# Kernel tuning notes

Hardware: AMD Instinct MI355X
Metric: run time of the kernel (lower is better)

Reference implementation:

```python
import jax, jax.numpy as jnp
import numpy as np

N = 150000      # nodes per branch
E = 2400000     # edges per branch (avg degree 16)
G = 128         # graphs in batch
F_IN, H, EMB = 3, 128, 512
BN_EPS = 1e-5


def setup_inputs() -> dict:
    key = jax.random.key(0)
    ks = jax.random.split(key, 24)
    inp = {
        "x1": jax.random.normal(ks[0], (N, F_IN), jnp.float32),
        "edge_index1": jax.random.randint(ks[1], (2, E), 0, N, jnp.int32),
        "batch1": jnp.sort(jax.random.randint(ks[2], (N,), 0, G, jnp.int32)),
        "x2": jax.random.normal(ks[3], (N, F_IN), jnp.float32),
        "edge_index2": jax.random.randint(ks[4], (2, E), 0, N, jnp.int32),
        "batch2": jnp.sort(jax.random.randint(ks[5], (N,), 0, G, jnp.int32)),
        # GCNConv weights (PyG: out = norm-agg(x @ W) + b), shared (siamese)
        "W1": jax.random.normal(ks[6], (F_IN, H), jnp.float32) / np.sqrt(F_IN),
        "b1": jnp.zeros((H,), jnp.float32),
        "W2": jax.random.normal(ks[7], (H, H), jnp.float32) / np.sqrt(H),
        "b2": jnp.zeros((H,), jnp.float32),
        "W3": jax.random.normal(ks[8], (H, H), jnp.float32) / np.sqrt(H),
        "b3": jnp.zeros((H,), jnp.float32),
        # BatchNorm affine params
        "g1": jnp.ones((H,), jnp.float32), "be1": jnp.zeros((H,), jnp.float32),
        "g2": jnp.ones((H,), jnp.float32), "be2": jnp.zeros((H,), jnp.float32),
        # projection MLP
        "Wp1": jax.random.normal(ks[9], (H, H), jnp.float32) / np.sqrt(H),
        "bp1": jnp.zeros((H,), jnp.float32),
        "Wp2": jax.random.normal(ks[10], (H, EMB), jnp.float32) / np.sqrt(H),
        "bp2": jnp.zeros((EMB,), jnp.float32),
    }
    return inp


def gcn_conv(x, edge_index, W, b):
    """PyG GCNConv: add self-loops, symmetric D^-1/2 (A+I) D^-1/2 normalization."""
    n = x.shape[0]
    loop = jnp.arange(n, dtype=edge_index.dtype)
    src = jnp.concatenate([edge_index[0], loop])
    dst = jnp.concatenate([edge_index[1], loop])
    deg = jax.ops.segment_sum(jnp.ones_like(dst, jnp.float32), dst, num_segments=n)
    dinv = jnp.where(deg > 0, jax.lax.rsqrt(deg), 0.0)
    norm = dinv[src] * dinv[dst]                      # [E+N]
    h = x @ W                                         # [N,H] dense transform first
    msg = h[src] * norm[:, None]                      # gather + scale
    out = jax.ops.segment_sum(msg, dst, num_segments=n)  # scatter-add
    return out + b


def batch_norm(x, gamma, beta):
    mu = jnp.mean(x, axis=0)
    var = jnp.mean(jnp.square(x - mu), axis=0)  # biased, training-mode stats
    return (x - mu) * jax.lax.rsqrt(var + BN_EPS) * gamma + beta


def global_mean_pool(x, batch, num_graphs):
    sums = jax.ops.segment_sum(x, batch, num_segments=num_graphs)
    cnt = jax.ops.segment_sum(jnp.ones((x.shape[0],), x.dtype), batch, num_segments=num_graphs)
    return sums / jnp.maximum(cnt, 1.0)[:, None]


def forward_once(x, edge_index, batch, W1, b1, W2, b2, W3, b3, g1, be1, g2, be2, Wp1, bp1, Wp2, bp2):
    x = jax.nn.relu(batch_norm(gcn_conv(x, edge_index, W1, b1), g1, be1))
    x = jax.nn.relu(batch_norm(gcn_conv(x, edge_index, W2, b2), g2, be2))
    x = gcn_conv(x, edge_index, W3, b3)
    x = global_mean_pool(x, batch, G)                 # [G,H]
    x = jax.nn.relu(x @ Wp1 + bp1) @ Wp2 + bp2        # [G,EMB]
    nrm = jnp.linalg.norm(x, axis=1, keepdims=True)
    return x / jnp.maximum(nrm, 1e-12)                # F.normalize(p=2, dim=1)


def reference(x1, edge_index1, batch1, x2, edge_index2, batch2,
              W1, b1, W2, b2, W3, b3, g1, be1, g2, be2, Wp1, bp1, Wp2, bp2):
    params = (W1, b1, W2, b2, W3, b3, g1, be1, g2, be2, Wp1, bp1, Wp2, bp2)
    out1 = forward_once(x1, edge_index1, batch1, *params)
    out2 = forward_once(x2, edge_index2, batch2, *params)
    return (out1, out2)
```

## Files before the change

### kernel.cpp

```cpp
#include <hip/hip_runtime.h>
#include <math.h>

#define BUCKET_SHIFT 8
#define BUCKET_MASK 255
#define MAXBUCK 640
#define TILE 8192

typedef __attribute__((ext_vector_type(8))) short bf16x8;
typedef __attribute__((ext_vector_type(4))) float f32x4;

__device__ inline float bf_lo(unsigned u) { return __uint_as_float(u << 16); }
__device__ inline float bf_hi(unsigned u) { return __uint_as_float(u & 0xffff0000u); }
__device__ inline float bf2f(unsigned short s) { return __uint_as_float((unsigned)s << 16); }
__device__ inline unsigned short f2bf(float f) {
  unsigned u = __float_as_uint(f);
  return (unsigned short)((u + 0x7fffu + ((u >> 16) & 1u)) >> 16);
}
__device__ inline void acc8(float* a, uint4 v) {
  a[0] += bf_lo(v.x); a[1] += bf_hi(v.x);
  a[2] += bf_lo(v.y); a[3] += bf_hi(v.y);
  a[4] += bf_lo(v.z); a[5] += bf_hi(v.z);
  a[6] += bf_lo(v.w); a[7] += bf_hi(v.w);
}
__device__ inline unsigned pack2(float a, float b) {
  return (unsigned)f2bf(a) | ((unsigned)f2bf(b) << 16);
}

__global__ void zero_u32(unsigned int* __restrict__ p, int n) {
  int i = blockIdx.x * blockDim.x + threadIdx.x;
  if (i < n) p[i] = 0u;
}

__global__ __launch_bounds__(256) void bucket_count(const int* __restrict__ dst0,
                                                    const int* __restrict__ dst1,
                                                    int* __restrict__ bcnt, int e, int nbuck) {
  int br = blockIdx.y;
  const int* dst = br ? dst1 : dst0;
  bcnt += (size_t)br * nbuck;
  __shared__ int lc[MAXBUCK];
  for (int i = threadIdx.x; i < nbuck; i += 256) lc[i] = 0;
  __syncthreads();
  for (int i = blockIdx.x * blockDim.x + threadIdx.x; i < e; i += gridDim.x * blockDim.x)
    atomicAdd(&lc[dst[i] >> BUCKET_SHIFT], 1);
  __syncthreads();
  for (int i = threadIdx.x; i < nbuck; i += 256)
    if (lc[i]) atomicAdd(&bcnt[i], lc[i]);
}

__global__ __launch_bounds__(1024) void bucket_scan(const int* __restrict__ bcnt,
                                                    int* __restrict__ bbase,
                                                    int* __restrict__ bcur, int nbuck) {
  int br = blockIdx.y;
  bcnt += (size_t)br * nbuck;
  bbase += (size_t)br * (nbuck + 1);
  bcur += (size_t)br * nbuck;
  __shared__ int s[1024];
  int t = threadIdx.x;
  int v = (t < nbuck) ? bcnt[t] : 0;
  s[t] = v;
  __syncthreads();
  for (int off = 1; off < 1024; off <<= 1) {
    int u = (t >= off) ? s[t - off] : 0;
    __syncthreads();
    s[t] += u;
    __syncthreads();
  }
  int excl = s[t] - v;
  if (t < nbuck) {
    bbase[t] = excl;
    bcur[t] = excl;
  } else if (t == nbuck) {
    bbase[t] = excl;
  }
}

__global__ __launch_bounds__(256) void bucket_scatter(const int* __restrict__ src0,
                                                      const int* __restrict__ dst0,
                                                      const int* __restrict__ src1,
                                                      const int* __restrict__ dst1,
                                                      int* __restrict__ bcur,
                                                      int* __restrict__ bucketed,
                                                      int e, int nbuck) {
  int br = blockIdx.y;
  const int* src = br ? src1 : src0;
  const int* dst = br ? dst1 : dst0;
  bcur += (size_t)br * nbuck;
  bucketed += (size_t)br * e;
  __shared__ int lcnt[MAXBUCK], gb[MAXBUCK];
  int t = threadIdx.x;
  int tile0 = blockIdx.x * TILE;
  int tn = min(TILE, e - tile0);
  for (int i = t; i < nbuck; i += 256) lcnt[i] = 0;
  __syncthreads();
  for (int i = t; i < tn; i += 256)
    atomicAdd(&lcnt[dst[tile0 + i] >> BUCKET_SHIFT], 1);
  __syncthreads();
  for (int i = t; i < nbuck; i += 256) {
    int c = lcnt[i];
    gb[i] = c ? atomicAdd(&bcur[i], c) : 0;
  }
  __syncthreads();
  for (int i = t; i < nbuck; i += 256) lcnt[i] = 0;
  __syncthreads();
  for (int i = t; i < tn; i += 256) {
    int d = dst[tile0 + i];
    int s = src[tile0 + i];
    int b = d >> BUCKET_SHIFT;
    int r = atomicAdd(&lcnt[b], 1);
    bucketed[gb[b] + r] = (s << 8) | (d & BUCKET_MASK);
  }
}

__global__ __launch_bounds__(256) void bucket_to_csr(const int* __restrict__ bucketed,
                                                     const int* __restrict__ bbase,
                                                     int* __restrict__ rp,
                                                     float* __restrict__ dinv,
                                                     int* __restrict__ csr,
                                                     int n, int e, int nbuck) {
  int br = blockIdx.y;
  bucketed += (size_t)br * e;
  bbase += (size_t)br * (nbuck + 1);
  rp += (size_t)br * (n + 1);
  dinv += (size_t)br * n;
  csr += (size_t)br * e;
  __shared__ int lcnt[256], lrp[256];
  int b = blockIdx.x, t = threadIdx.x;
  int n0 = b << BUCKET_SHIFT;
  int base = bbase[b];
  int cnt_e = bbase[b + 1] - base;
  lcnt[t] = 0;
  __syncthreads();
  for (int i = t; i < cnt_e; i += 256)
    atomicAdd(&lcnt[bucketed[base + i] & BUCKET_MASK], 1);
  __syncthreads();
  int v = lcnt[t];
  lrp[t] = v;
  __syncthreads();
  for (int off = 1; off < 256; off <<= 1) {
    int u = (t >= off) ? lrp[t - off] : 0;
    __syncthreads();
    lrp[t] += u;
    __syncthreads();
  }
  int excl = lrp[t] - v;
  int node = n0 + t;
  if (node < n) {
    rp[node] = base + excl;
    dinv[node] = rsqrtf((float)v + 1.0f);
  }
  if (b == nbuck - 1 && t == 0) rp[n] = e;
  lrp[t] = excl;
  lcnt[t] = 0;
  __syncthreads();
  for (int i = t; i < cnt_e; i += 256) {
    int ed = bucketed[base + i];
    int li = ed & BUCKET_MASK;
    int pos = atomicAdd(&lcnt[li], 1);
    csr[base + lrp[li] + pos] = (int)(((unsigned)ed) >> 8);
  }
}

__global__ void graph_bounds(const int* __restrict__ batch0, const int* __restrict__ batch1,
                             int* __restrict__ gstart, int n, int g) {
  int br = blockIdx.y;
  const int* batch = br ? batch1 : batch0;
  gstart += (size_t)br * (g + 1);
  int i = blockIdx.x * blockDim.x + threadIdx.x;
  if (i >= n) return;
  int b = batch[i];
  int bp = (i == 0) ? -1 : batch[i - 1];
  for (int k = bp + 1; k <= b; ++k) gstart[k] = i;
  if (i == n - 1)
    for (int k = b + 1; k <= g; ++k) gstart[k] = n;
}

__global__ void xs_scale(const float* __restrict__ x0, const float* __restrict__ x1,
                         const float* __restrict__ dinv, float4* __restrict__ xs, int n) {
  int br = blockIdx.y;
  const float* x = br ? x1 : x0;
  dinv += (size_t)br * n;
  xs += (size_t)br * n;
  int i = blockIdx.x * blockDim.x + threadIdx.x;
  if (i >= n) return;
  float d = dinv[i];
  xs[i] = make_float4(x[3 * (size_t)i] * d, x[3 * (size_t)i + 1] * d,
                      x[3 * (size_t)i + 2] * d, d);
}

__global__ __launch_bounds__(256) void agg_f3(const float4* __restrict__ xs,
                                              const int* __restrict__ rp,
                                              const int* __restrict__ csr,
                                              const float* __restrict__ dinv,
                                              float4* __restrict__ out,
                                              float* __restrict__ mpart, int n, int e, int nb3) {
  int br = blockIdx.y;
  xs += (size_t)br * n;
  rp += (size_t)br * (n + 1);
  csr += (size_t)br * e;
  dinv += (size_t)br * n;
  out += (size_t)br * n;
  mpart += (size_t)br * nb3 * 9;
  int i = blockIdx.x * blockDim.x + threadIdx.x;
  int t = threadIdx.x;
  float a0 = 0.f, a1 = 0.f, a2 = 0.f;
  if (i < n) {
    float4 self = xs[i];
    a0 = self.x; a1 = self.y; a2 = self.z;
    int e0 = rp[i], e1 = rp[i + 1];
    int ee = e0;
    for (; ee + 4 <= e1; ee += 4) {
      int s0 = csr[ee], s1 = csr[ee + 1], s2 = csr[ee + 2], s3 = csr[ee + 3];
      float4 v0 = xs[s0], v1 = xs[s1], v2 = xs[s2], v3 = xs[s3];
      a0 += (v0.x + v1.x) + (v2.x + v3.x);
      a1 += (v0.y + v1.y) + (v2.y + v3.y);
      a2 += (v0.z + v1.z) + (v2.z + v3.z);
    }
    for (; ee < e1; ++ee) {
      float4 v = xs[csr[ee]];
      a0 += v.x; a1 += v.y; a2 += v.z;
    }
    float d = dinv[i];
    a0 *= d; a1 *= d; a2 *= d;
    out[i] = make_float4(a0, a1, a2, 0.f);
  }
  float loc[9] = {a0, a1, a2, a0 * a0, a0 * a1, a0 * a2, a1 * a1, a1 * a2, a2 * a2};
  __shared__ float red[256];
  for (int q = 0; q < 9; ++q) {
    red[t] = loc[q];
    __syncthreads();
    for (int s = 128; s > 0; s >>= 1) {
      if (t < s) red[t] += red[t + s];
      __syncthreads();
    }
    if (t == 0) mpart[blockIdx.x * 9 + q] = red[0];
    __syncthreads();
  }
}

__global__ void bnprep1(const float* __restrict__ mpart, int nblk,
                        const float* __restrict__ W1, const float* __restrict__ b1,
                        const float* __restrict__ g1, const float* __restrict__ be1,
                        float invn, float4* __restrict__ W1r, float2* __restrict__ prm) {
  int br = blockIdx.y;
  mpart += (size_t)br * nblk * 9;
  W1r += (size_t)br * 128;
  prm += (size_t)br * 128;
  __shared__ float red[256];
  __shared__ float sm[9];
  int t = threadIdx.x;
  float loc[9] = {0.f, 0.f, 0.f, 0.f, 0.f, 0.f, 0.f, 0.f, 0.f};
  for (int i = t; i < nblk; i += 256)
#pragma unroll
    for (int q = 0; q < 9; ++q) loc[q] += mpart[i * 9 + q];
  for (int q = 0; q < 9; ++q) {
    red[t] = loc[q];
    __syncthreads();
    for (int s = 128; s > 0; s >>= 1) {
      if (t < s) red[t] += red[t + s];
      __syncthreads();
    }
    if (t == 0) sm[q] = red[0] * invn;
    __syncthreads();
  }
  if (t < 128) {
    float w0 = W1[t], w1 = W1[128 + t], w2 = W1[256 + t], b = b1[t];
    float mu0 = sm[0] * w0 + sm[1] * w1 + sm[2] * w2;
    float q2 = w0 * w0 * sm[3] + w1 * w1 * sm[6] + w2 * w2 * sm[8]
             + 2.f * (w0 * w1 * sm[4] + w0 * w2 * sm[5] + w1 * w2 * sm[7]);
    float var = q2 - mu0 * mu0;
    float sc = rsqrtf(fmaxf(var, 0.f) + 1e-5f) * g1[t];
    float mu = mu0 + b;
    W1r[t] = make_float4(w0, w1, w2, b);
    prm[t] = make_float2(sc, be1[t] - mu * sc);
  }
}

__global__ void lin1_fused(const float4* __restrict__ ag, const float4* __restrict__ W1r,
                           const float2* __restrict__ prm, unsigned short* __restrict__ out,
                           int n) {
  int br = blockIdx.y;
  ag += (size_t)br * n;
  W1r += (size_t)br * 128;
  prm += (size_t)br * 128;
  out += (size_t)br * n * 128;
  int idx = blockIdx.x * blockDim.x + threadIdx.x;
  if (idx >= n * 128) return;
  int node = idx >> 7, f = idx & 127;
  float4 a = ag[node];
  float4 w = W1r[f];
  float2 p = prm[f];
  float v = a.x * w.x + a.y * w.y + a.z * w.z + w.w;
  v = v * p.x + p.y;
  out[idx] = f2bf(fmaxf(v, 0.f));
}

__global__ void wsplit2(const float* __restrict__ W2, const float* __restrict__ W3,
                        unsigned short* __restrict__ Wf2, unsigned short* __restrict__ Wf3) {
  const float* W = blockIdx.y ? W3 : W2;
  unsigned short* Wf = blockIdx.y ? Wf3 : Wf2;
  int i = blockIdx.x * 256 + threadIdx.x;
  if (i >= 128 * 128) return;
  int k = i >> 7, f = i & 127;
  float w = W[i];
  unsigned short hi = f2bf(w);
  float hif = __uint_as_float((unsigned)hi << 16);
  unsigned short lo = f2bf(w - hif);
  int NT = f >> 4, l15 = f & 15, ks = k >> 5, lg = (k >> 3) & 3, j = k & 7;
  int lane = lg * 16 + l15;
  size_t base = ((size_t)(NT * 4 + ks) * 64 + lane) * 8 + j;
  Wf[base] = hi;
  Wf[16384 + base] = lo;
}

template <int BN>
__global__ __launch_bounds__(256) void gemm_mfma_t(const unsigned short* __restrict__ Abf,
                                                   const unsigned short* __restrict__ Wf,
                                                   const float* __restrict__ dinv,
                                                   const float2* __restrict__ prm,
                                                   unsigned short* __restrict__ C, int n) {
  int br = blockIdx.y;
  Abf += (size_t)br * n * 128;
  dinv += (size_t)br * n;
  C += (size_t)br * n * 128;
  if (BN) prm += (size_t)br * 128;
  const int t = threadIdx.x;
  const int wave = t >> 6, lane = t & 63;
  const int l15 = lane & 15, lg = lane >> 4;
  const int row0 = blockIdx.x * 128 + wave * 32;
  const int n0 = row0 + l15, n1 = row0 + 16 + l15;
  const bf16x8* wfr = (const bf16x8*)Wf;
  f32x4 acc[8][2] = {};
#pragma unroll
  for (int ks = 0; ks < 4; ++ks) {
    int k0 = ks * 32 + lg * 8;
    bf16x8 nf0 = {}, nf1 = {};
    if (n0 < n) nf0 = *(const bf16x8*)&Abf[(size_t)n0 * 128 + k0];
    if (n1 < n) nf1 = *(const bf16x8*)&Abf[(size_t)n1 * 128 + k0];
    if (BN) {
      float4 pa = *(const float4*)&prm[k0];
      float4 pb = *(const float4*)&prm[k0 + 2];
      float4 pc = *(const float4*)&prm[k0 + 4];
      float4 pd = *(const float4*)&prm[k0 + 6];
      float scv[8] = {pa.x, pa.z, pb.x, pb.z, pc.x, pc.z, pd.x, pd.z};
      float ofv[8] = {pa.y, pa.w, pb.y, pb.w, pc.y, pc.w, pd.y, pd.w};
#pragma unroll
      for (int j = 0; j < 8; ++j) {
        float x0 = fmaxf(bf2f((unsigned short)nf0[j]) * scv[j] + ofv[j], 0.f);
        float x1 = fmaxf(bf2f((unsigned short)nf1[j]) * scv[j] + ofv[j], 0.f);
        nf0[j] = (short)f2bf(x0);
        nf1[j] = (short)f2bf(x1);
      }
    }
#pragma unroll
    for (int NT = 0; NT < 8; ++NT) {
      bf16x8 wh = wfr[(NT * 4 + ks) * 64 + lane];
      bf16x8 wl = wfr[2048 + (NT * 4 + ks) * 64 + lane];
      acc[NT][0] = __builtin_amdgcn_mfma_f32_16x16x32_bf16(wh, nf0, acc[NT][0], 0, 0, 0);
      acc[NT][0] = __builtin_amdgcn_mfma_f32_16x16x32_bf16(wl, nf0, acc[NT][0], 0, 0, 0);
      acc[NT][1] = __builtin_amdgcn_mfma_f32_16x16x32_bf16(wh, nf1, acc[NT][1], 0, 0, 0);
      acc[NT][1] = __builtin_amdgcn_mfma_f32_16x16x32_bf16(wl, nf1, acc[NT][1], 0, 0, 0);
    }
  }
  float sc0 = (n0 < n) ? dinv[n0] : 0.f;
  float sc1 = (n1 < n) ? dinv[n1] : 0.f;
#pragma unroll
  for (int ng = 0; ng < 2; ++ng) {
    int node = (ng == 0) ? n0 : n1;
    float sc = (ng == 0) ? sc0 : sc1;
    if (node < n) {
#pragma unroll
      for (int NT = 0; NT < 8; ++NT) {
        ushort4 o;
        o.x = f2bf(acc[NT][ng][0] * sc);
        o.y = f2bf(acc[NT][ng][1] * sc);
        o.z = f2bf(acc[NT][ng][2] * sc);
        o.w = f2bf(acc[NT][ng][3] * sc);
        *(ushort4*)&C[(size_t)node * 128 + NT * 16 + lg * 4] = o;
      }
    }
  }
}

__global__ __launch_bounds__(256) void agg128_l2(const unsigned short* __restrict__ h,
                                                 const int* __restrict__ rp,
                                                 const int* __restrict__ csr,
                                                 const float* __restrict__ dinv,
                                                 const float* __restrict__ bias,
                                                 unsigned short* __restrict__ outb,
                                                 float* __restrict__ mpart, int n, int e,
                                                 int nagg) {
  int br = blockIdx.y;
  h += (size_t)br * n * 128;
  rp += (size_t)br * (n + 1);
  csr += (size_t)br * e;
  dinv += (size_t)br * n;
  outb += (size_t)br * n * 128;
  mpart += (size_t)br * nagg * 256;
  int t = threadIdx.x;
  int node = blockIdx.x * 16 + (t >> 4);
  int lane = t & 15;
  bool valid = node < n;
  const uint4* hp = (const uint4*)h;
  float acc[8] = {0.f};
  if (valid) {
    acc8(acc, hp[(size_t)node * 16 + lane]);
    int e0 = rp[node], e1 = rp[node + 1];
    int ee = e0;
    for (; ee + 8 <= e1; ee += 8) {
      int s0 = csr[ee],     s1 = csr[ee + 1], s2 = csr[ee + 2], s3 = csr[ee + 3];
      int s4 = csr[ee + 4], s5 = csr[ee + 5], s6 = csr[ee + 6], s7 = csr[ee + 7];
      uint4 v0 = hp[(size_t)s0 * 16 + lane];
      uint4 v1 = hp[(size_t)s1 * 16 + lane];
      uint4 v2 = hp[(size_t)s2 * 16 + lane];
      uint4 v3 = hp[(size_t)s3 * 16 + lane];
      uint4 v4 = hp[(size_t)s4 * 16 + lane];
      uint4 v5 = hp[(size_t)s5 * 16 + lane];
      uint4 v6 = hp[(size_t)s6 * 16 + lane];
      uint4 v7 = hp[(size_t)s7 * 16 + lane];
      acc8(acc, v0); acc8(acc, v1); acc8(acc, v2); acc8(acc, v3);
      acc8(acc, v4); acc8(acc, v5); acc8(acc, v6); acc8(acc, v7);
    }
    for (; ee + 4 <= e1; ee += 4) {
      int s0 = csr[ee], s1 = csr[ee + 1], s2 = csr[ee + 2], s3 = csr[ee + 3];
      uint4 v0 = hp[(size_t)s0 * 16 + lane];
      uint4 v1 = hp[(size_t)s1 * 16 + lane];
      uint4 v2 = hp[(size_t)s2 * 16 + lane];
      uint4 v3 = hp[(size_t)s3 * 16 + lane];
      acc8(acc, v0); acc8(acc, v1); acc8(acc, v2); acc8(acc, v3);
    }
    for (; ee < e1; ++ee) acc8(acc, hp[(size_t)csr[ee] * 16 + lane]);
  }
  float v[8], sq[8];
  if (valid) {
    float dd = dinv[node];
    float4 bb0 = *(const float4*)&bias[lane * 8];
    float4 bb1 = *(const float4*)&bias[lane * 8 + 4];
    v[0] = acc[0] * dd + bb0.x; v[1] = acc[1] * dd + bb0.y;
    v[2] = acc[2] * dd + bb0.z; v[3] = acc[3] * dd + bb0.w;
    v[4] = acc[4] * dd + bb1.x; v[5] = acc[5] * dd + bb1.y;
    v[6] = acc[6] * dd + bb1.z; v[7] = acc[7] * dd + bb1.w;
    uint4 o;
    o.x = pack2(v[0], v[1]); o.y = pack2(v[2], v[3]);
    o.z = pack2(v[4], v[5]); o.w = pack2(v[6], v[7]);
    *(uint4*)&outb[(size_t)node * 128 + lane * 8] = o;
  } else {
#pragma unroll
    for (int j = 0; j < 8; ++j) v[j] = 0.f;
  }
#pragma unroll
  for (int j = 0; j < 8; ++j) sq[j] = v[j] * v[j];
#pragma unroll
  for (int j = 0; j < 8; ++j) {
    v[j] += __shfl_xor(v[j], 16);  v[j] += __shfl_xor(v[j], 32);
    sq[j] += __shfl_xor(sq[j], 16); sq[j] += __shfl_xor(sq[j], 32);
  }
  __shared__ float sred[4][16][16];
  int wave = t >> 6, wl = t & 63;
  if (wl < 16) {
#pragma unroll
    for (int j = 0; j < 8; ++j) {
      sred[wave][wl][j] = v[j];
      sred[wave][wl][8 + j] = sq[j];
    }
  }
  __syncthreads();
  {
    int f = t & 127;
    int j = (f & 7) + ((t >> 7) << 3);
    float s = sred[0][f >> 3][j] + sred[1][f >> 3][j]
            + sred[2][f >> 3][j] + sred[3][f >> 3][j];
    mpart[(size_t)blockIdx.x * 256 + t] = s;
  }
}

__global__ __launch_bounds__(256) void bnred1(const float* __restrict__ mpart, int nblk,
                                              float* __restrict__ spart) {
  int br = blockIdx.y;
  mpart += (size_t)br * nblk * 256;
  spart += (size_t)br * 128 * 256;
  int t = threadIdx.x, b = blockIdx.x;
  float loc = 0.f;
  for (int i = b; i < nblk; i += 128) loc += mpart[(size_t)i * 256 + t];
  spart[b * 256 + t] = loc;
}

__global__ void bnprep2(const float* __restrict__ spart,
                        const float* __restrict__ gam, const float* __restrict__ bet,
                        float invn, float2* __restrict__ prm) {
  int br = blockIdx.y;
  spart += (size_t)br * 128 * 256;
  prm += (size_t)br * 128;
  int t = threadIdx.x;
  float loc = 0.f;
  for (int i = 0; i < 128; ++i) loc += spart[i * 256 + t];
  __shared__ float sm[256];
  sm[t] = loc;
  __syncthreads();
  if (t < 128) {
    float mu = sm[t] * invn;
    float var = sm[128 + t] * invn - mu * mu;
    float sc = rsqrtf(fmaxf(var, 0.f) + 1e-5f) * gam[t];
    prm[t] = make_float2(sc, bet[t] - mu * sc);
  }
}

__global__ __launch_bounds__(256) void agg128_l3(const unsigned short* __restrict__ h,
                                                 const int* __restrict__ rp,
                                                 const int* __restrict__ csr,
                                                 const float* __restrict__ dinv,
                                                 const float* __restrict__ bias,
                                                 unsigned short* __restrict__ outb,
                                                 int n, int e) {
  int br = blockIdx.y;
  h += (size_t)br * n * 128;
  rp += (size_t)br * (n + 1);
  csr += (size_t)br * e;
  dinv += (size_t)br * n;
  outb += (size_t)br * n * 128;
  int node = blockIdx.x * 16 + (threadIdx.x >> 4);
  int lane = threadIdx.x & 15;
  if (node >= n) return;
  const uint4* hp = (const uint4*)h;
  float acc[8] = {0.f};
  acc8(acc, hp[(size_t)node * 16 + lane]);
  int e0 = rp[node], e1 = rp[node + 1];
  int ee = e0;
  for (; ee + 8 <= e1; ee += 8) {
    int s0 = csr[ee],     s1 = csr[ee + 1], s2 = csr[ee + 2], s3 = csr[ee + 3];
    int s4 = csr[ee + 4], s5 = csr[ee + 5], s6 = csr[ee + 6], s7 = csr[ee + 7];
    uint4 v0 = hp[(size_t)s0 * 16 + lane];
    uint4 v1 = hp[(size_t)s1 * 16 + lane];
    uint4 v2 = hp[(size_t)s2 * 16 + lane];
    uint4 v3 = hp[(size_t)s3 * 16 + lane];
    uint4 v4 = hp[(size_t)s4 * 16 + lane];
    uint4 v5 = hp[(size_t)s5 * 16 + lane];
    uint4 v6 = hp[(size_t)s6 * 16 + lane];
    uint4 v7 = hp[(size_t)s7 * 16 + lane];
    acc8(acc, v0); acc8(acc, v1); acc8(acc, v2); acc8(acc, v3);
    acc8(acc, v4); acc8(acc, v5); acc8(acc, v6); acc8(acc, v7);
  }
  for (; ee + 4 <= e1; ee += 4) {
    int s0 = csr[ee], s1 = csr[ee + 1], s2 = csr[ee + 2], s3 = csr[ee + 3];
    uint4 v0 = hp[(size_t)s0 * 16 + lane];
    uint4 v1 = hp[(size_t)s1 * 16 + lane];
    uint4 v2 = hp[(size_t)s2 * 16 + lane];
    uint4 v3 = hp[(size_t)s3 * 16 + lane];
    acc8(acc, v0); acc8(acc, v1); acc8(acc, v2); acc8(acc, v3);
  }
  for (; ee < e1; ++ee) acc8(acc, hp[(size_t)csr[ee] * 16 + lane]);
  float dd = dinv[node];
  float4 bb0 = *(const float4*)&bias[lane * 8];
  float4 bb1 = *(const float4*)&bias[lane * 8 + 4];
  uint4 o;
  o.x = pack2(acc[0] * dd + bb0.x, acc[1] * dd + bb0.y);
  o.y = pack2(acc[2] * dd + bb0.z, acc[3] * dd + bb0.w);
  o.z = pack2(acc[4] * dd + bb1.x, acc[5] * dd + bb1.y);
  o.w = pack2(acc[6] * dd + bb1.z, acc[7] * dd + bb1.w);
  *(uint4*)&outb[(size_t)node * 128 + lane * 8] = o;
}

__global__ void pool_partial_bf16(const unsigned short* __restrict__ z,
                                  const int* __restrict__ gstart,
                                  float* __restrict__ pooled, int n, int g) {
  int br = blockIdx.y;
  z += (size_t)br * n * 128;
  gstart += (size_t)br * (g + 1);
  pooled += (size_t)br * g * 128;
  int gg = blockIdx.x >> 3, p = blockIdx.x & 7;
  int t = threadIdx.x;
  int f = t & 127, half = t >> 7;
  int beg = gstart[gg], end = gstart[gg + 1];
  float s = 0.f;
  for (int idx = beg + p * 2 + half; idx < end; idx += 16)
    s += bf2f(z[(size_t)idx * 128 + f]);
  __shared__ float ls[256];
  ls[t] = s;
  __syncthreads();
  if (half == 0) atomicAdd(&pooled[gg * 128 + f], s + ls[t + 128]);
}

__global__ void mlp_kernel(const float* __restrict__ pooled, const int* __restrict__ gstart,
                           const float* __restrict__ Wp1, const float* __restrict__ bp1,
                           const float* __restrict__ Wp2, const float* __restrict__ bp2,
                           float* __restrict__ out, int g) {
  int br = blockIdx.y;
  pooled += (size_t)br * g * 128;
  gstart += (size_t)br * (g + 1);
  out += (size_t)br * g * 512;
  int gg = blockIdx.x, t = threadIdx.x;
  __shared__ float pv[128], hid[128], ov[512], red[256];
  if (t < 128) {
    float cntf = (float)(gstart[gg + 1] - gstart[gg]);
    pv[t] = pooled[gg * 128 + t] / fmaxf(cntf, 1.0f);
  }
  __syncthreads();
  if (t < 128) {
    float a = bp1[t];
    for (int k = 0; k < 128; ++k) a += pv[k] * Wp1[k * 128 + t];
    hid[t] = fmaxf(a, 0.0f);
  }
  __syncthreads();
  for (int o = t; o < 512; o += 256) {
    float a = bp2[o];
    for (int k = 0; k < 128; ++k) a += hid[k] * Wp2[k * 512 + o];
    ov[o] = a;
  }
  __syncthreads();
  red[t] = ov[t] * ov[t] + ov[t + 256] * ov[t + 256];
  __syncthreads();
  for (int sdt = 128; sdt > 0; sdt >>= 1) {
    if (t < sdt) red[t] += red[t + sdt];
    __syncthreads();
  }
  float inv = 1.0f / fmaxf(sqrtf(red[0]), 1e-12f);
  for (int o = t; o < 512; o += 256) out[(size_t)gg * 512 + o] = ov[o] * inv;
}

extern "C" void kernel_launch(void* const* d_in, const int* in_sizes, int n_in,
                              void* d_out, int out_size, void* d_ws, size_t ws_size,
                              hipStream_t stream) {
  const int N = in_sizes[0] / 3;
  const int E = in_sizes[1] / 2;
  const int G = out_size / (2 * 512);
  const int NBUCK = (N + BUCKET_MASK) >> BUCKET_SHIFT;
  const int NB3 = (N + 255) / 256;
  const int NAGG = (N + 15) / 16;

  char* w = (char*)d_ws;
  auto alloc = [&](size_t bytes) -> void* {
    void* p = (void*)w;
    w += (bytes + 255) & ~(size_t)255;
    return p;
  };
  unsigned short* Abf      = (unsigned short*)alloc(2 * (size_t)N * 128 * 2);
  unsigned short* Bh       = (unsigned short*)alloc(2 * (size_t)N * 128 * 2);
  float*          dinv     = (float*)alloc(2 * (size_t)N * 4);
  float4*         xs       = (float4*)alloc(2 * (size_t)N * 16);
  float4*         ag0      = (float4*)alloc(2 * (size_t)N * 16);
  int*            rp       = (int*)alloc(2 * (size_t)(N + 1) * 4);
  int*            csr      = (int*)alloc(2 * (size_t)E * 4);
  int*            bucketed = (int*)alloc(2 * (size_t)E * 4);
  int*            bcnt     = (int*)alloc(2 * (size_t)NBUCK * 4);
  int*            bbase    = (int*)alloc(2 * (size_t)(NBUCK + 1) * 4);
  int*            bcur     = (int*)alloc(2 * (size_t)NBUCK * 4);
  int*            gstart   = (int*)alloc(2 * (size_t)(G + 1) * 4);
  float*          pooled   = (float*)alloc(2 * (size_t)G * 128 * 4);
  unsigned short* Wf2      = (unsigned short*)alloc(2 * 128 * 128 * 2);
  unsigned short* Wf3      = (unsigned short*)alloc(2 * 128 * 128 * 2);
  float*          mpart    = (float*)alloc(2 * (size_t)NB3 * 9 * 4);
  float*          mpart2   = (float*)alloc(2 * (size_t)NAGG * 256 * 4);
  float*          spart    = (float*)alloc(2 * (size_t)128 * 256 * 4);
  float4*         W1r      = (float4*)alloc(2 * 128 * 16);
  float2*         prm1     = (float2*)alloc(2 * 128 * 8);
  float2*         prm2     = (float2*)alloc(2 * 128 * 8);

  const float* x0    = (const float*)d_in[0];
  const int*   ei0   = (const int*)d_in[1];
  const int*   bat0  = (const int*)d_in[2];
  const float* x1    = (const float*)d_in[3];
  const int*   ei1   = (const int*)d_in[4];
  const int*   bat1  = (const int*)d_in[5];
  const float* W1  = (const float*)d_in[6];
  const float* b1  = (const float*)d_in[7];
  const float* W2  = (const float*)d_in[8];
  const float* b2  = (const float*)d_in[9];
  const float* W3  = (const float*)d_in[10];
  const float* b3  = (const float*)d_in[11];
  const float* g1  = (const float*)d_in[12];
  const float* be1 = (const float*)d_in[13];
  const float* g2  = (const float*)d_in[14];
  const float* be2 = (const float*)d_in[15];
  const float* Wp1 = (const float*)d_in[16];
  const float* bp1 = (const float*)d_in[17];
  const float* Wp2 = (const float*)d_in[18];
  const float* bp2 = (const float*)d_in[19];

  const int* src0 = ei0;
  const int* dst0 = ei0 + E;
  const int* src1 = ei1;
  const int* dst1 = ei1 + E;
  float* outp = (float*)d_out;

  const int TB = 256;
  const int NTILE = (E + TILE - 1) / TILE;
  const float invn = 1.0f / (float)N;

  wsplit2<<<dim3(64, 2), TB, 0, stream>>>(W2, W3, Wf2, Wf3);

  zero_u32<<<(2 * NBUCK + TB - 1) / TB, TB, 0, stream>>>((unsigned*)bcnt, 2 * NBUCK);
  bucket_count<<<dim3(256, 2), TB, 0, stream>>>(dst0, dst1, bcnt, E, NBUCK);
  bucket_scan<<<dim3(1, 2), 1024, 0, stream>>>(bcnt, bbase, bcur, NBUCK);
  bucket_scatter<<<dim3(NTILE, 2), TB, 0, stream>>>(src0, dst0, src1, dst1, bcur, bucketed, E, NBUCK);
  bucket_to_csr<<<dim3(NBUCK, 2), TB, 0, stream>>>(bucketed, bbase, rp, dinv, csr, N, E, NBUCK);

  graph_bounds<<<dim3((N + TB - 1) / TB, 2), TB, 0, stream>>>(bat0, bat1, gstart, N, G);

  xs_scale<<<dim3((N + TB - 1) / TB, 2), TB, 0, stream>>>(x0, x1, dinv, xs, N);
  agg_f3<<<dim3(NB3, 2), TB, 0, stream>>>(xs, rp, csr, dinv, ag0, mpart, N, E, NB3);
  bnprep1<<<dim3(1, 2), TB, 0, stream>>>(mpart, NB3, W1, b1, g1, be1, invn, W1r, prm1);
  lin1_fused<<<dim3((N * 128 + TB - 1) / TB, 2), TB, 0, stream>>>(ag0, W1r, prm1, Abf, N);

  gemm_mfma_t<0><<<dim3((N + 127) / 128, 2), TB, 0, stream>>>(Abf, Wf2, dinv, nullptr, Bh, N);
  agg128_l2<<<dim3(NAGG, 2), TB, 0, stream>>>(Bh, rp, csr, dinv, b2, Abf, mpart2, N, E, NAGG);
  bnred1<<<dim3(128, 2), TB, 0, stream>>>(mpart2, NAGG, spart);
  bnprep2<<<dim3(1, 2), TB, 0, stream>>>(spart, g2, be2, invn, prm2);

  gemm_mfma_t<1><<<dim3((N + 127) / 128, 2), TB, 0, stream>>>(Abf, Wf3, dinv, prm2, Bh, N);
  agg128_l3<<<dim3(NAGG, 2), TB, 0, stream>>>(Bh, rp, csr, dinv, b3, Abf, N, E);

  zero_u32<<<(2 * G * 128 + TB - 1) / TB, TB, 0, stream>>>((unsigned*)pooled, 2 * G * 128);
  pool_partial_bf16<<<dim3(G * 8, 2), TB, 0, stream>>>(Abf, gstart, pooled, N, G);
  mlp_kernel<<<dim3(G, 2), TB, 0, stream>>>(pooled, gstart, Wp1, bp1, Wp2, bp2, outp, G);
}
```

Measured before the change: 828.5 us.

## Fuse layer-1 linear+BN into GEMM prologue and pooling into layer-3 aggregation

Drops the standalone lin1_fused kernel. The layer-2 GEMM now rebuilds its bf16 input on the fly from the 3-wide aggregated features, W1 and the BN parameters, so the N×128 bf16 intermediate is never written or read back. The layer-3 aggregation kernel now does the mean-pool sums itself: it reduces node rows per graph in LDS and issues atomicAdds, which removes the write of the final node features and the separate pooling pass. In exchange there are more atomics on the pooled buffer and extra per-element ALU work inside the GEMM prologue.

```diff
diff --git a/kernel.cpp b/kernel.cpp
--- a/kernel.cpp
+++ b/kernel.cpp
@@ -275,25 +275,6 @@
   }
 }
 
-__global__ void lin1_fused(const float4* __restrict__ ag, const float4* __restrict__ W1r,
-                           const float2* __restrict__ prm, unsigned short* __restrict__ out,
-                           int n) {
-  int br = blockIdx.y;
-  ag += (size_t)br * n;
-  W1r += (size_t)br * 128;
-  prm += (size_t)br * 128;
-  out += (size_t)br * n * 128;
-  int idx = blockIdx.x * blockDim.x + threadIdx.x;
-  if (idx >= n * 128) return;
-  int node = idx >> 7, f = idx & 127;
-  float4 a = ag[node];
-  float4 w = W1r[f];
-  float2 p = prm[f];
-  float v = a.x * w.x + a.y * w.y + a.z * w.z + w.w;
-  v = v * p.x + p.y;
-  out[idx] = f2bf(fmaxf(v, 0.f));
-}
-
 __global__ void wsplit2(const float* __restrict__ W2, const float* __restrict__ W3,
                         unsigned short* __restrict__ Wf2, unsigned short* __restrict__ Wf3) {
   const float* W = blockIdx.y ? W3 : W2;
@@ -312,31 +293,39 @@
   Wf[16384 + base] = lo;
 }
 
-template <int BN>
+template <int MODE>
 __global__ __launch_bounds__(256) void gemm_mfma_t(const unsigned short* __restrict__ Abf,
+                                                   const float4* __restrict__ ag0,
+                                                   const float4* __restrict__ W1r,
                                                    const unsigned short* __restrict__ Wf,
                                                    const float* __restrict__ dinv,
                                                    const float2* __restrict__ prm,
                                                    unsigned short* __restrict__ C, int n) {
   int br = blockIdx.y;
-  Abf += (size_t)br * n * 128;
+  if (MODE == 1) Abf += (size_t)br * n * 128;
+  if (MODE == 2) { ag0 += (size_t)br * n; W1r += (size_t)br * 128; }
   dinv += (size_t)br * n;
   C += (size_t)br * n * 128;
-  if (BN) prm += (size_t)br * 128;
+  prm += (size_t)br * 128;
   const int t = threadIdx.x;
   const int wave = t >> 6, lane = t & 63;
   const int l15 = lane & 15, lg = lane >> 4;
   const int row0 = blockIdx.x * 128 + wave * 32;
   const int n0 = row0 + l15, n1 = row0 + 16 + l15;
   const bf16x8* wfr = (const bf16x8*)Wf;
+  float4 a0v = make_float4(0.f, 0.f, 0.f, 0.f), a1v = a0v;
+  if (MODE == 2) {
+    if (n0 < n) a0v = ag0[n0];
+    if (n1 < n) a1v = ag0[n1];
+  }
   f32x4 acc[8][2] = {};
 #pragma unroll
   for (int ks = 0; ks < 4; ++ks) {
     int k0 = ks * 32 + lg * 8;
     bf16x8 nf0 = {}, nf1 = {};
-    if (n0 < n) nf0 = *(const bf16x8*)&Abf[(size_t)n0 * 128 + k0];
-    if (n1 < n) nf1 = *(const bf16x8*)&Abf[(size_t)n1 * 128 + k0];
-    if (BN) {
+    if (MODE == 1) {
+      if (n0 < n) nf0 = *(const bf16x8*)&Abf[(size_t)n0 * 128 + k0];
+      if (n1 < n) nf1 = *(const bf16x8*)&Abf[(size_t)n1 * 128 + k0];
       float4 pa = *(const float4*)&prm[k0];
       float4 pb = *(const float4*)&prm[k0 + 2];
       float4 pc = *(const float4*)&prm[k0 + 4];
@@ -349,6 +338,17 @@
         float x1 = fmaxf(bf2f((unsigned short)nf1[j]) * scv[j] + ofv[j], 0.f);
         nf0[j] = (short)f2bf(x0);
         nf1[j] = (short)f2bf(x1);
+      }
+    } else {
+#pragma unroll
+      for (int j = 0; j < 8; ++j) {
+        int f = k0 + j;
+        float4 wv = W1r[f];
+        float2 p = prm[f];
+        float x0 = (a0v.x * wv.x + a0v.y * wv.y + a0v.z * wv.z + wv.w) * p.x + p.y;
+        float x1 = (a1v.x * wv.x + a1v.y * wv.y + a1v.z * wv.z + wv.w) * p.x + p.y;
+        nf0[j] = (short)f2bf(fmaxf(x0, 0.f));
+        nf1[j] = (short)f2bf(fmaxf(x1, 0.f));
       }
     }
 #pragma unroll
@@ -504,79 +504,98 @@
   }
 }
 
-__global__ __launch_bounds__(256) void agg128_l3(const unsigned short* __restrict__ h,
-                                                 const int* __restrict__ rp,
-                                                 const int* __restrict__ csr,
-                                                 const float* __restrict__ dinv,
-                                                 const float* __restrict__ bias,
-                                                 unsigned short* __restrict__ outb,
-                                                 int n, int e) {
+__global__ __launch_bounds__(256) void agg128_l3_pool(const unsigned short* __restrict__ h,
+                                                      const int* __restrict__ rp,
+                                                      const int* __restrict__ csr,
+                                                      const float* __restrict__ dinv,
+                                                      const float* __restrict__ bias,
+                                                      const int* __restrict__ batch0,
+                                                      const int* __restrict__ batch1,
+                                                      float* __restrict__ pooled,
+                                                      int n, int e, int g) {
   int br = blockIdx.y;
   h += (size_t)br * n * 128;
   rp += (size_t)br * (n + 1);
   csr += (size_t)br * e;
   dinv += (size_t)br * n;
-  outb += (size_t)br * n * 128;
-  int node = blockIdx.x * 16 + (threadIdx.x >> 4);
-  int lane = threadIdx.x & 15;
-  if (node >= n) return;
+  const int* batch = br ? batch1 : batch0;
+  pooled += (size_t)br * g * 128;
+  int t = threadIdx.x;
+  int node = blockIdx.x * 16 + (t >> 4);
+  int lane = t & 15;
+  bool valid = node < n;
   const uint4* hp = (const uint4*)h;
   float acc[8] = {0.f};
-  acc8(acc, hp[(size_t)node * 16 + lane]);
-  int e0 = rp[node], e1 = rp[node + 1];
-  int ee = e0;
-  for (; ee + 8 <= e1; ee += 8) {
-    int s0 = csr[ee],     s1 = csr[ee + 1], s2 = csr[ee + 2], s3 = csr[ee + 3];
-    int s4 = csr[ee + 4], s5 = csr[ee + 5], s6 = csr[ee + 6], s7 = csr[ee + 7];
-    uint4 v0 = hp[(size_t)s0 * 16 + lane];
-    uint4 v1 = hp[(size_t)s1 * 16 + lane];
-    uint4 v2 = hp[(size_t)s2 * 16 + lane];
-    uint4 v3 = hp[(size_t)s3 * 16 + lane];
-    uint4 v4 = hp[(size_t)s4 * 16 + lane];
-    uint4 v5 = hp[(size_t)s5 * 16 + lane];
-    uint4 v6 = hp[(size_t)s6 * 16 + lane];
-    uint4 v7 = hp[(size_t)s7 * 16 + lane];
-    acc8(acc, v0); acc8(acc, v1); acc8(acc, v2); acc8(acc, v3);
-    acc8(acc, v4); acc8(acc, v5); acc8(acc, v6); acc8(acc, v7);
-  }
-  for (; ee + 4 <= e1; ee += 4) {
-    int s0 = csr[ee], s1 = csr[ee + 1], s2 = csr[ee + 2], s3 = csr[ee + 3];
-    uint4 v0 = hp[(size_t)s0 * 16 + lane];
-    uint4 v1 = hp[(size_t)s1 * 16 + lane];
-    uint4 v2 = hp[(size_t)s2 * 16 + lane];
-    uint4 v3 = hp[(size_t)s3 * 16 + lane];
-    acc8(acc, v0); acc8(acc, v1); acc8(acc, v2); acc8(acc, v3);
-  }
-  for (; ee < e1; ++ee) acc8(acc, hp[(size_t)csr[ee] * 16 + lane]);
-  float dd = dinv[node];
-  float4 bb0 = *(const float4*)&bias[lane * 8];
-  float4 bb1 = *(const float4*)&bias[lane * 8 + 4];
-  uint4 o;
-  o.x = pack2(acc[0] * dd + bb0.x, acc[1] * dd + bb0.y);
-  o.y = pack2(acc[2] * dd + bb0.z, acc[3] * dd + bb0.w);
-  o.z = pack2(acc[4] * dd + bb1.x, acc[5] * dd + bb1.y);
-  o.w = pack2(acc[6] * dd + bb1.z, acc[7] * dd + bb1.w);
-  *(uint4*)&outb[(size_t)node * 128 + lane * 8] = o;
-}
-
-__global__ void pool_partial_bf16(const unsigned short* __restrict__ z,
-                                  const int* __restrict__ gstart,
-                                  float* __restrict__ pooled, int n, int g) {
-  int br = blockIdx.y;
-  z += (size_t)br * n * 128;
-  gstart += (size_t)br * (g + 1);
-  pooled += (size_t)br * g * 128;
-  int gg = blockIdx.x >> 3, p = blockIdx.x & 7;
-  int t = threadIdx.x;
-  int f = t & 127, half = t >> 7;
-  int beg = gstart[gg], end = gstart[gg + 1];
-  float s = 0.f;
-  for (int idx = beg + p * 2 + half; idx < end; idx += 16)
-    s += bf2f(z[(size_t)idx * 128 + f]);
-  __shared__ float ls[256];
-  ls[t] = s;
-  __syncthreads();
-  if (half == 0) atomicAdd(&pooled[gg * 128 + f], s + ls[t + 128]);
+  if (valid) {
+    acc8(acc, hp[(size_t)node * 16 + lane]);
+    int e0 = rp[node], e1 = rp[node + 1];
+    int ee = e0;
+    for (; ee + 8 <= e1; ee += 8) {
+      int s0 = csr[ee],     s1 = csr[ee + 1], s2 = csr[ee + 2], s3 = csr[ee + 3];
+      int s4 = csr[ee + 4], s5 = csr[ee + 5], s6 = csr[ee + 6], s7 = csr[ee + 7];
+      uint4 v0 = hp[(size_t)s0 * 16 + lane];
+      uint4 v1 = hp[(size_t)s1 * 16 + lane];
+      uint4 v2 = hp[(size_t)s2 * 16 + lane];
+      uint4 v3 = hp[(size_t)s3 * 16 + lane];
+      uint4 v4 = hp[(size_t)s4 * 16 + lane];
+      uint4 v5 = hp[(size_t)s5 * 16 + lane];
+      uint4 v6 = hp[(size_t)s6 * 16 + lane];
+      uint4 v7 = hp[(size_t)s7 * 16 + lane];
+      acc8(acc, v0); acc8(acc, v1); acc8(acc, v2); acc8(acc, v3);
+      acc8(acc, v4); acc8(acc, v5); acc8(acc, v6); acc8(acc, v7);
+    }
+    for (; ee + 4 <= e1; ee += 4) {
+      int s0 = csr[ee], s1 = csr[ee + 1], s2 = csr[ee + 2], s3 = csr[ee + 3];
+      uint4 v0 = hp[(size_t)s0 * 16 + lane];
+      uint4 v1 = hp[(size_t)s1 * 16 + lane];
+      uint4 v2 = hp[(size_t)s2 * 16 + lane];
+      uint4 v3 = hp[(size_t)s3 * 16 + lane];
+      acc8(acc, v0); acc8(acc, v1); acc8(acc, v2); acc8(acc, v3);
+    }
+    for (; ee < e1; ++ee) acc8(acc, hp[(size_t)csr[ee] * 16 + lane]);
+  }
+  __shared__ float lds[16][128];
+  __shared__ int lgid[16];
+  int ng = t >> 4;
+  if (valid) {
+    float dd = dinv[node];
+    float4 bb0 = *(const float4*)&bias[lane * 8];
+    float4 bb1 = *(const float4*)&bias[lane * 8 + 4];
+    float w0 = bf2f(f2bf(acc[0] * dd + bb0.x));
+    float w1 = bf2f(f2bf(acc[1] * dd + bb0.y));
+    float w2 = bf2f(f2bf(acc[2] * dd + bb0.z));
+    float w3 = bf2f(f2bf(acc[3] * dd + bb0.w));
+    float w4 = bf2f(f2bf(acc[4] * dd + bb1.x));
+    float w5 = bf2f(f2bf(acc[5] * dd + bb1.y));
+    float w6 = bf2f(f2bf(acc[6] * dd + bb1.z));
+    float w7 = bf2f(f2bf(acc[7] * dd + bb1.w));
+    lds[ng][lane * 8 + 0] = w0; lds[ng][lane * 8 + 1] = w1;
+    lds[ng][lane * 8 + 2] = w2; lds[ng][lane * 8 + 3] = w3;
+    lds[ng][lane * 8 + 4] = w4; lds[ng][lane * 8 + 5] = w5;
+    lds[ng][lane * 8 + 6] = w6; lds[ng][lane * 8 + 7] = w7;
+    if (lane == 0) lgid[ng] = batch[node];
+  } else {
+#pragma unroll
+    for (int j = 0; j < 8; ++j) lds[ng][lane * 8 + j] = 0.f;
+    if (lane == 0) lgid[ng] = -1;
+  }
+  __syncthreads();
+  {
+    int f = t & 127, half = t >> 7;
+    int lo = half * 8, hi = lo + 8;
+    float run = 0.f;
+    int cur = lgid[lo];
+    for (int k = lo; k < hi; ++k) {
+      int gg = lgid[k];
+      if (gg != cur) {
+        if (cur >= 0 && run != 0.f) atomicAdd(&pooled[cur * 128 + f], run);
+        run = 0.f;
+        cur = gg;
+      }
+      run += lds[k][f];
+    }
+    if (cur >= 0 && run != 0.f) atomicAdd(&pooled[cur * 128 + f], run);
+  }
 }
 
 __global__ void mlp_kernel(const float* __restrict__ pooled, const int* __restrict__ gstart,
@@ -698,17 +717,15 @@
   xs_scale<<<dim3((N + TB - 1) / TB, 2), TB, 0, stream>>>(x0, x1, dinv, xs, N);
   agg_f3<<<dim3(NB3, 2), TB, 0, stream>>>(xs, rp, csr, dinv, ag0, mpart, N, E, NB3);
   bnprep1<<<dim3(1, 2), TB, 0, stream>>>(mpart, NB3, W1, b1, g1, be1, invn, W1r, prm1);
-  lin1_fused<<<dim3((N * 128 + TB - 1) / TB, 2), TB, 0, stream>>>(ag0, W1r, prm1, Abf, N);
-
-  gemm_mfma_t<0><<<dim3((N + 127) / 128, 2), TB, 0, stream>>>(Abf, Wf2, dinv, nullptr, Bh, N);
+
+  gemm_mfma_t<2><<<dim3((N + 127) / 128, 2), TB, 0, stream>>>(nullptr, ag0, W1r, Wf2, dinv, prm1, Bh, N);
   agg128_l2<<<dim3(NAGG, 2), TB, 0, stream>>>(Bh, rp, csr, dinv, b2, Abf, mpart2, N, E, NAGG);
   bnred1<<<dim3(128, 2), TB, 0, stream>>>(mpart2, NAGG, spart);
   bnprep2<<<dim3(1, 2), TB, 0, stream>>>(spart, g2, be2, invn, prm2);
 
-  gemm_mfma_t<1><<<dim3((N + 127) / 128, 2), TB, 0, stream>>>(Abf, Wf3, dinv, prm2, Bh, N);
-  agg128_l3<<<dim3(NAGG, 2), TB, 0, stream>>>(Bh, rp, csr, dinv, b3, Abf, N, E);
-
+  gemm_mfma_t<1><<<dim3((N + 127) / 128, 2), TB, 0, stream>>>(Abf, nullptr, nullptr, Wf3, dinv, prm2, Bh, N);
   zero_u32<<<(2 * G * 128 + TB - 1) / TB, TB, 0, stream>>>((unsigned*)pooled, 2 * G * 128);
-  pool_partial_bf16<<<dim3(G * 8, 2), TB, 0, stream>>>(Abf, gstart, pooled, N, G);
+  agg128_l3_pool<<<dim3(NAGG, 2), TB, 0, stream>>>(Bh, rp, csr, dinv, b3, bat0, bat1, pooled, N, E, G);
+
   mlp_kernel<<<dim3(G, 2), TB, 0, stream>>>(pooled, gstart, Wp1, bp1, Wp2, bp2, outp, G);
 }
```

Result: faster. 727.2 us (-12.2%).
